# Performance work log

Measured on AMD Instinct MI355X. Metric: run time of the kernel, lower is better.

The kernel has to match this reference:

```python
import jax, jax.numpy as jnp
import numpy as np

M1, M2, M3 = 16, 16, 3  # Fourier mode truncation (modes3 hard-coded to 3 in torch __init__)


def setup_inputs() -> dict:
    key = jax.random.key(0)
    k0, k1, k2, k3, k4 = jax.random.split(key, 5)
    B, Ci, Co, T, X, P = 8, 32, 32, 128, 256, 3
    scale = 1.0 / (Ci * Co)
    x = jax.random.normal(k0, (B, Ci, T, X, P), dtype=jnp.float32)
    w1_re = scale * jax.random.uniform(k1, (Ci, Co, M1, M2, M3), dtype=jnp.float32)
    w1_im = scale * jax.random.uniform(k2, (Ci, Co, M1, M2, M3), dtype=jnp.float32)
    w2_re = scale * jax.random.uniform(k3, (Ci, Co, M1, M2, M3), dtype=jnp.float32)
    w2_im = scale * jax.random.uniform(k4, (Ci, Co, M1, M2, M3), dtype=jnp.float32)
    return {"x": x, "w1_re": w1_re, "w1_im": w1_im, "w2_re": w2_re, "w2_im": w2_im}


def reference(x, w1_re, w1_im, w2_re, w2_im):
    # x: [B, Ci, T, X, P] -- pipes pre-stacked along last dim (method == 34 branch)
    B, Ci, T, X, P = x.shape
    Co = w1_re.shape[1]
    w1 = (w1_re + 1j * w1_im).astype(jnp.complex64)
    w2 = (w2_re + 1j * w2_im).astype(jnp.complex64)

    x_ft = jnp.fft.rfftn(x, axes=(2, 3, 4))          # [B, Ci, T, X, P//2+1]
    z = min(x_ft.shape[4], M3)                       # torch: z_dim = min(x_ft.shape[4], modes3)

    # low-x / low-y corner
    coeff1 = jnp.zeros((B, Ci, M1, M2, M3), jnp.complex64)
    coeff1 = coeff1.at[..., :z].set(x_ft[:, :, :M1, :M2, :z])
    blk1 = jnp.einsum('bixyz,ioxyz->boxyz', coeff1, w1)

    # high-x / low-y corner
    coeff2 = jnp.zeros((B, Ci, M1, M2, M3), jnp.complex64)
    coeff2 = coeff2.at[..., :z].set(x_ft[:, :, -M1:, :M2, :z])
    blk2 = jnp.einsum('bixyz,ioxyz->boxyz', coeff2, w2)

    out_ft = jnp.zeros((B, Co, T, X, P), jnp.complex64)
    out_ft = out_ft.at[:, :, :M1, :M2, :M3].set(blk1)
    out_ft = out_ft.at[:, :, -M1:, :M2, :M3].set(blk2)

    # irfftn with s=(T, X, P) crops last axis to P//2+1 coeffs, matching torch semantics
    out = jnp.fft.irfftn(out_ft, s=(T, X, P), axes=(-3, -2, -1))  # [B, Co, T, X, P] float32
    return out
```

## Files before the change

### kernel.cpp

```cpp
#include <hip/hip_runtime.h>
#include <math.h>

typedef float2 F2;

__device__ __forceinline__ F2 cmul(F2 a, F2 b) {
    return make_float2(a.x * b.x - a.y * b.y, a.x * b.y + a.y * b.x);
}
__device__ __forceinline__ F2 cmac(F2 acc, F2 a, F2 b) {
    acc.x += a.x * b.x - a.y * b.y;
    acc.y += a.x * b.y + a.y * b.x;
    return acc;
}

#define TWO_PI 6.283185307179586f
#define SQRT3_2 0.8660254037844386f
#define SQRT3 1.7320508075688772f

__device__ constexpr float TW16X[16] = {
    1.f,  0.923879533f,  0.707106781f,  0.382683432f,  0.f, -0.382683432f,
    -0.707106781f, -0.923879533f, -1.f, -0.923879533f, -0.707106781f,
    -0.382683432f, 0.f,  0.382683432f,  0.707106781f,  0.923879533f};
__device__ constexpr float TW16Y[16] = {
    0.f, -0.382683432f, -0.707106781f, -0.923879533f, -1.f, -0.923879533f,
    -0.707106781f, -0.382683432f, 0.f,  0.382683432f,  0.707106781f,
    0.923879533f,  1.f,  0.923879533f,  0.707106781f,  0.382683432f};

__global__ __launch_bounds__(256) void k1_fwd_x(const float* __restrict__ x,
                                                F2* __restrict__ y) {
    __shared__ float xp0[8][260];
    __shared__ F2    xp1[8][260];
    __shared__ F2    tw[256];
    __shared__ F2    part[1024];
    const int tid = threadIdx.x;
    const int blk = blockIdx.x;

    {
        float sv, cv;
        sincosf(-TWO_PI * (float)tid * (1.0f / 256.0f), &sv, &cv);
        tw[tid] = make_float2(cv, sv);
    }
#pragma unroll
    for (int j = 0; j < 8; ++j) {
        int item = tid + 256 * j;
        int row = item >> 8, xx = item & 255;
        const float* src = x + ((size_t)(blk * 8 + row) * 256 + xx) * 3;
        float a = src[0], b = src[1], c = src[2];
        xp0[row][xx] = a + b + c;
        xp1[row][xx] = make_float2(a - 0.5f * (b + c), SQRT3_2 * (c - b));
    }
    __syncthreads();

    const int kz = tid >> 7, rr = (tid >> 4) & 7, kxg = (tid >> 2) & 3, c = tid & 3;
    const float sgn = (kxg & 1) ? -1.0f : 1.0f;

    const F2 c01 = tw[(32 * kxg) & 255];
    const F2 c02 = tw[(64 * kxg) & 255];
    const F2 c03 = tw[(96 * kxg) & 255];
    const F2 f1 = tw[(4 * c) & 255];
    const F2 f2 = tw[(8 * c) & 255];
    const F2 f3 = tw[(12 * c) & 255];

    F2 T0[8], T1[8];
    if (kz == 0) {
        const float* r0 = xp0[rr];
#pragma unroll
        for (int b = 0; b < 8; ++b) {
            int x0 = c + 4 * b;
            float s0 = fmaf(sgn, r0[x0 + 128], r0[x0]);
            float s1 = fmaf(sgn, r0[x0 + 160], r0[x0 + 32]);
            float s2 = fmaf(sgn, r0[x0 + 192], r0[x0 + 64]);
            float s3 = fmaf(sgn, r0[x0 + 224], r0[x0 + 96]);
            F2 p1 = make_float2(s1 * c01.x, s1 * c01.y);
            F2 p2 = make_float2(s2 * c02.x, s2 * c02.y);
            F2 p3 = make_float2(s3 * c03.x, s3 * c03.y);
            T0[b] = make_float2(s0 + p1.x + p2.x + p3.x, p1.y + p2.y + p3.y);
            T1[b] = make_float2(s0 - p1.x + p2.x - p3.x, -p1.y + p2.y - p3.y);
        }
    } else {
        const F2* r1 = xp1[rr];
#pragma unroll
        for (int b = 0; b < 8; ++b) {
            int x0 = c + 4 * b;
            F2 a0 = r1[x0],      b0 = r1[x0 + 128];
            F2 a1 = r1[x0 + 32], b1 = r1[x0 + 160];
            F2 a2 = r1[x0 + 64], b2 = r1[x0 + 192];
            F2 a3 = r1[x0 + 96], b3 = r1[x0 + 224];
            F2 s0 = make_float2(fmaf(sgn, b0.x, a0.x), fmaf(sgn, b0.y, a0.y));
            F2 s1 = make_float2(fmaf(sgn, b1.x, a1.x), fmaf(sgn, b1.y, a1.y));
            F2 s2 = make_float2(fmaf(sgn, b2.x, a2.x), fmaf(sgn, b2.y, a2.y));
            F2 s3 = make_float2(fmaf(sgn, b3.x, a3.x), fmaf(sgn, b3.y, a3.y));
            F2 p1 = cmul(s1, c01);
            F2 p2 = cmul(s2, c02);
            F2 p3 = cmul(s3, c03);
            T0[b] = make_float2(s0.x + p1.x + p2.x + p3.x, s0.y + p1.y + p2.y + p3.y);
            T1[b] = make_float2(s0.x - p1.x + p2.x - p3.x, s0.y - p1.y + p2.y - p3.y);
        }
    }

    F2 acc0 = make_float2(0.f, 0.f), acc1 = acc0, acc2 = acc0, acc3 = acc0;
#pragma unroll
    for (int b = 0; b < 8; ++b) {
        F2 tb = tw[(kxg * (c + 4 * b)) & 255];
        F2 q0 = cmul(tb, T0[b]);
        F2 q1 = cmul(tb, T1[b]);
        acc0.x += q0.x; acc0.y += q0.y;
        {
            const float Cx = TW16X[(2 * b) & 15], Cy = TW16Y[(2 * b) & 15];
            acc2.x += q0.x * Cx - q0.y * Cy;
            acc2.y += q0.x * Cy + q0.y * Cx;
        }
        {
            const float Cx = TW16X[b & 15], Cy = TW16Y[b & 15];
            acc1.x += q1.x * Cx - q1.y * Cy;
            acc1.y += q1.x * Cy + q1.y * Cx;
        }
        {
            const float Cx = TW16X[(3 * b) & 15], Cy = TW16Y[(3 * b) & 15];
            acc3.x += q1.x * Cx - q1.y * Cy;
            acc3.y += q1.x * Cy + q1.y * Cx;
        }
    }
    acc1 = cmul(acc1, f1);
    acc2 = cmul(acc2, f2);
    acc3 = cmul(acc3, f3);

    {
        const int base = (((rr * 2 + kz) * 16 + kxg) << 2) + c;
        part[base]       = acc0;
        part[base + 16]  = acc1;
        part[base + 32]  = acc2;
        part[base + 48]  = acc3;
    }
    __syncthreads();
    {
        int rr2 = tid >> 5, kz2 = (tid >> 4) & 1, kx2 = tid & 15;
        const F2* p = &part[((rr2 * 2 + kz2) * 16 + kx2) << 2];
        F2 r = p[0];
        r.x += p[1].x + p[2].x + p[3].x;
        r.y += p[1].y + p[2].y + p[3].y;
        y[((size_t)(blk * 8 + rr2) * 2 + kz2) * 16 + kx2] = r;
    }
}

__global__ __launch_bounds__(256) void k2a_fwd_t(const F2* __restrict__ y,
                                                 F2* __restrict__ xft) {
    __shared__ F2 yL[128][16];
    const int tid = threadIdx.x;
    const int bi = blockIdx.x >> 1, kz = blockIdx.x & 1;
#pragma unroll
    for (int j = 0; j < 8; ++j) {
        int item = tid + 256 * j;
        int t = item >> 4, kx = item & 15;
        yL[t][kx] = y[((size_t)(bi * 128 + t) * 2 + kz) * 16 + kx];
    }
    __syncthreads();

    const int kx = tid & 15, sg = tid >> 4;
    F2 rotA = make_float2(1.f, 0.f), rotB = make_float2(1.f, 0.f), stepA, stepB;
    sincosf(-TWO_PI * (float)sg * (1.0f / 128.0f), &stepA.y, &stepA.x);
    sincosf(-TWO_PI * (float)(112 + sg) * (1.0f / 128.0f), &stepB.y, &stepB.x);
    F2 accA = make_float2(0.f, 0.f), accB = make_float2(0.f, 0.f);
#pragma unroll 8
    for (int t = 0; t < 128; ++t) {
        F2 v = yL[t][kx];
        accA = cmac(accA, v, rotA);
        accB = cmac(accB, v, rotB);
        rotA = cmul(rotA, stepA);
        rotB = cmul(rotB, stepB);
    }
    const int b = bi >> 5, i = bi & 31;
    xft[(((size_t)(b * 32 + sg) * 2 + kz) * 16 + kx) * 32 + i] = accA;
    xft[(((size_t)(b * 32 + (16 + sg)) * 2 + kz) * 16 + kx) * 32 + i] = accB;
}

__global__ __launch_bounds__(256) void k2b_mix(const F2* __restrict__ xft,
                                               const float* __restrict__ w1re,
                                               const float* __restrict__ w1im,
                                               const float* __restrict__ w2re,
                                               const float* __restrict__ w2im,
                                               F2* __restrict__ blkout) {
    __shared__ F2 xL[512];
    __shared__ F2 wcL[2][32][32];
    const int tid = threadIdx.x;
    const int s = blockIdx.x >> 4, kx = blockIdx.x & 15;
#pragma unroll
    for (int j = 0; j < 2; ++j) {
        int item = tid + 256 * j;
        int b = item >> 6, kz = (item >> 5) & 1, i = item & 31;
        xL[item] = xft[(((size_t)(b * 32 + s) * 2 + kz) * 16 + kx) * 32 + i];
    }
    const float* bre = (s < 16) ? w1re : w2re;
    const float* bim = (s < 16) ? w1im : w2im;
    const int m1 = s & 15;
#pragma unroll
    for (int j = 0; j < 4; ++j) {
        int iop = tid + 256 * j;
        int i = iop >> 5, o = iop & 31;
        size_t g = (((size_t)(i * 32 + o) * 16 + m1) * 16 + kx) * 3;
        wcL[0][i][o] = make_float2(bre[g], bim[g]);
        wcL[1][i][o] = make_float2(bre[g + 1], bim[g + 1]);
    }
    __syncthreads();

    const int b = tid >> 5, o = tid & 31;
#pragma unroll
    for (int kz = 0; kz < 2; ++kz) {
        F2 acc = make_float2(0.f, 0.f);
#pragma unroll 8
        for (int i = 0; i < 32; ++i) {
            F2 xv = xL[(b * 2 + kz) * 32 + i];
            F2 wv = wcL[kz][i][o];
            acc.x += xv.x * wv.x - xv.y * wv.y;
            acc.y += xv.x * wv.y + xv.y * wv.x;
        }
        blkout[(((size_t)(b * 32 + o) * 32 + s) * 2 + kz) * 16 + kx] = acc;
    }
}

__global__ __launch_bounds__(256) void k2c_inv_t(const F2* __restrict__ blkin,
                                                 F2* __restrict__ h) {
    __shared__ F2 bL[1024];
    const int tid = threadIdx.x;
    const int bo = blockIdx.x >> 2, tc = blockIdx.x & 3;
#pragma unroll
    for (int j = 0; j < 4; ++j) {
        int item = tid + 256 * j;
        bL[item] = blkin[(size_t)bo * 1024 + item];
    }
    __syncthreads();

    const int col = tid & 31, tl = tid >> 5;
    F2 accA[4], accB[4], w[4], stp[4];
#pragma unroll
    for (int q = 0; q < 4; ++q) {
        accA[q] = make_float2(0.f, 0.f);
        accB[q] = make_float2(0.f, 0.f);
        w[q] = make_float2(1.f, 0.f);
        int t = 32 * tc + tl + 8 * q;
        sincosf(TWO_PI * (float)t * (1.0f / 128.0f), &stp[q].y, &stp[q].x);
    }
#pragma unroll 4
    for (int sp = 0; sp < 16; ++sp) {
        F2 bA = bL[sp * 32 + col];
        F2 bB = bL[(16 + sp) * 32 + col];
#pragma unroll
        for (int q = 0; q < 4; ++q) {
            accA[q] = cmac(accA[q], bA, w[q]);
            accB[q] = cmac(accB[q], bB, w[q]);
            w[q] = cmul(w[q], stp[q]);
        }
    }
    F2 phase;
    sincosf(-TWO_PI * (float)tl * (1.0f / 8.0f), &phase.y, &phase.x);
#pragma unroll
    for (int q = 0; q < 4; ++q) {
        int t = 32 * tc + tl + 8 * q;
        F2 r = cmac(accA[q], phase, accB[q]);
        h[((size_t)bo * 128 + t) * 32 + col] = r;
    }
}

__global__ __launch_bounds__(256) void k3_inv_x(const F2* __restrict__ h,
                                                float* __restrict__ out) {
    __shared__ F2 hL[64];
    __shared__ float oL[1536];
    const int tid = threadIdx.x;
    const int blk = blockIdx.x;
    if (tid < 64) hL[tid] = h[(size_t)blk * 64 + tid];
    __syncthreads();

    const int rr = tid >> 7, x = tid & 127;
    const F2* hrow = &hL[rr * 32];
    F2 w = make_float2(1.f, 0.f), r;
    sincosf(TWO_PI * (float)x * (1.0f / 256.0f), &r.y, &r.x);
    float e0 = 0.f, o0 = 0.f;
    F2 e1 = make_float2(0.f, 0.f), o1 = make_float2(0.f, 0.f);
#pragma unroll
    for (int k2 = 0; k2 < 8; ++k2) {
        {
            F2 h0 = hrow[2 * k2], h1 = hrow[16 + 2 * k2];
            e0 += h0.x * w.x - h0.y * w.y;
            e1.x += h1.x * w.x - h1.y * w.y;
            e1.y += h1.x * w.y + h1.y * w.x;
            w = cmul(w, r);
        }
        {
            F2 h0 = hrow[2 * k2 + 1], h1 = hrow[16 + 2 * k2 + 1];
            o0 += h0.x * w.x - h0.y * w.y;
            o1.x += h1.x * w.x - h1.y * w.y;
            o1.y += h1.x * w.y + h1.y * w.x;
            w = cmul(w, r);
        }
    }
    const float n = 1.0f / 98304.0f;
    float* o = &oL[rr * 768];
    {
        float g0 = e0 + o0, g1r = e1.x + o1.x, g1i = e1.y + o1.y;
        o[x * 3 + 0] = n * (g0 + 2.f * g1r);
        o[x * 3 + 1] = n * (g0 - g1r - SQRT3 * g1i);
        o[x * 3 + 2] = n * (g0 - g1r + SQRT3 * g1i);
    }
    {
        float g0 = e0 - o0, g1r = e1.x - o1.x, g1i = e1.y - o1.y;
        int xb = x + 128;
        o[xb * 3 + 0] = n * (g0 + 2.f * g1r);
        o[xb * 3 + 1] = n * (g0 - g1r - SQRT3 * g1i);
        o[xb * 3 + 2] = n * (g0 - g1r + SQRT3 * g1i);
    }
    __syncthreads();
    {
        float4* dst = (float4*)(out + (size_t)blk * 1536);
        const float4* src = (const float4*)oL;
        dst[tid] = src[tid];
        if (tid < 128) dst[tid + 256] = src[tid + 256];
    }
}

extern "C" void kernel_launch(void* const* d_in, const int* in_sizes, int n_in,
                              void* d_out, int out_size, void* d_ws, size_t ws_size,
                              hipStream_t stream) {
    const float* x    = (const float*)d_in[0];
    const float* w1re = (const float*)d_in[1];
    const float* w1im = (const float*)d_in[2];
    const float* w2re = (const float*)d_in[3];
    const float* w2im = (const float*)d_in[4];
    float* out = (float*)d_out;

    F2* y   = (F2*)d_ws;
    F2* xft = y + 1048576;
    F2* bk  = xft + 262144;
    F2* h   = bk + 262144;

    hipLaunchKernelGGL(k1_fwd_x,  dim3(4096),  dim3(256), 0, stream, x, y);
    hipLaunchKernelGGL(k2a_fwd_t, dim3(512),   dim3(256), 0, stream, y, xft);
    hipLaunchKernelGGL(k2b_mix,   dim3(512),   dim3(256), 0, stream, xft,
                       w1re, w1im, w2re, w2im, bk);
    hipLaunchKernelGGL(k2c_inv_t, dim3(1024),  dim3(256), 0, stream, bk, h);
    hipLaunchKernelGGL(k3_inv_x,  dim3(16384), dim3(256), 0, stream, h, out);
}
```

Measured before the change: 253.7 us.

## Fuse inverse T-DFT and inverse X/P-DFT kernels through shared memory

Merges the inverse time-axis DFT kernel and the inverse x/p-axis kernel into one kernel. The intermediate h tile stays in shared memory instead of making a round trip through global memory, and one launch is dropped. Each block now produces 32 time rows in four rounds, with extra syncs between rounds. The grid drops from 16384 small blocks to 1024 blocks, and shared memory use rises to about 40KB per block, which may lower occupancy.

```diff
diff --git a/kernel.cpp b/kernel.cpp
--- a/kernel.cpp
+++ b/kernel.cpp
@@ -217,11 +217,14 @@
     }
 }
 
-__global__ __launch_bounds__(256) void k2c_inv_t(const F2* __restrict__ blkin,
-                                                 F2* __restrict__ h) {
+__global__ __launch_bounds__(256) void k23_inv_tx(const F2* __restrict__ blkin,
+                                                  float* __restrict__ out) {
     __shared__ F2 bL[1024];
+    __shared__ F2 hT[32][32];
+    __shared__ __align__(16) float oL[8][768];
     const int tid = threadIdx.x;
     const int bo = blockIdx.x >> 2, tc = blockIdx.x & 3;
+
 #pragma unroll
     for (int j = 0; j < 4; ++j) {
         int item = tid + 256 * j;
@@ -229,90 +232,88 @@
     }
     __syncthreads();
 
-    const int col = tid & 31, tl = tid >> 5;
-    F2 accA[4], accB[4], w[4], stp[4];
-#pragma unroll
-    for (int q = 0; q < 4; ++q) {
-        accA[q] = make_float2(0.f, 0.f);
-        accB[q] = make_float2(0.f, 0.f);
-        w[q] = make_float2(1.f, 0.f);
-        int t = 32 * tc + tl + 8 * q;
-        sincosf(TWO_PI * (float)t * (1.0f / 128.0f), &stp[q].y, &stp[q].x);
-    }
+    {
+        const int col = tid & 31, tl = tid >> 5;
+        F2 accA[4], accB[4], w[4], stp[4];
+#pragma unroll
+        for (int q = 0; q < 4; ++q) {
+            accA[q] = make_float2(0.f, 0.f);
+            accB[q] = make_float2(0.f, 0.f);
+            w[q] = make_float2(1.f, 0.f);
+            int t = 32 * tc + tl + 8 * q;
+            sincosf(TWO_PI * (float)t * (1.0f / 128.0f), &stp[q].y, &stp[q].x);
+        }
 #pragma unroll 4
-    for (int sp = 0; sp < 16; ++sp) {
-        F2 bA = bL[sp * 32 + col];
-        F2 bB = bL[(16 + sp) * 32 + col];
+        for (int sp = 0; sp < 16; ++sp) {
+            F2 bA = bL[sp * 32 + col];
+            F2 bB = bL[(16 + sp) * 32 + col];
+#pragma unroll
+            for (int q = 0; q < 4; ++q) {
+                accA[q] = cmac(accA[q], bA, w[q]);
+                accB[q] = cmac(accB[q], bB, w[q]);
+                w[q] = cmul(w[q], stp[q]);
+            }
+        }
+        F2 phase;
+        sincosf(-TWO_PI * (float)tl * (1.0f / 8.0f), &phase.y, &phase.x);
 #pragma unroll
         for (int q = 0; q < 4; ++q) {
-            accA[q] = cmac(accA[q], bA, w[q]);
-            accB[q] = cmac(accB[q], bB, w[q]);
-            w[q] = cmul(w[q], stp[q]);
-        }
-    }
-    F2 phase;
-    sincosf(-TWO_PI * (float)tl * (1.0f / 8.0f), &phase.y, &phase.x);
-#pragma unroll
-    for (int q = 0; q < 4; ++q) {
-        int t = 32 * tc + tl + 8 * q;
-        F2 r = cmac(accA[q], phase, accB[q]);
-        h[((size_t)bo * 128 + t) * 32 + col] = r;
-    }
-}
-
-__global__ __launch_bounds__(256) void k3_inv_x(const F2* __restrict__ h,
-                                                float* __restrict__ out) {
-    __shared__ F2 hL[64];
-    __shared__ float oL[1536];
-    const int tid = threadIdx.x;
-    const int blk = blockIdx.x;
-    if (tid < 64) hL[tid] = h[(size_t)blk * 64 + tid];
-    __syncthreads();
-
-    const int rr = tid >> 7, x = tid & 127;
-    const F2* hrow = &hL[rr * 32];
-    F2 w = make_float2(1.f, 0.f), r;
-    sincosf(TWO_PI * (float)x * (1.0f / 256.0f), &r.y, &r.x);
-    float e0 = 0.f, o0 = 0.f;
-    F2 e1 = make_float2(0.f, 0.f), o1 = make_float2(0.f, 0.f);
-#pragma unroll
-    for (int k2 = 0; k2 < 8; ++k2) {
+            hT[tl + 8 * q][col] = cmac(accA[q], phase, accB[q]);
+        }
+    }
+    __syncthreads();
+
+    const int xg = tid & 31, tl2 = tid >> 5;
+    const float n = 1.0f / 98304.0f;
+    for (int rd = 0; rd < 4; ++rd) {
+        const F2* hrow = &hT[rd * 8 + tl2][0];
+        float* o = oL[tl2];
+#pragma unroll
+        for (int j = 0; j < 4; ++j) {
+            const int x = xg + 32 * j;
+            F2 w = make_float2(1.f, 0.f), r;
+            sincosf(TWO_PI * (float)x * (1.0f / 256.0f), &r.y, &r.x);
+            float e0 = 0.f, o0 = 0.f;
+            F2 e1 = make_float2(0.f, 0.f), o1 = make_float2(0.f, 0.f);
+#pragma unroll
+            for (int k2 = 0; k2 < 8; ++k2) {
+                {
+                    F2 h0 = hrow[2 * k2], h1 = hrow[16 + 2 * k2];
+                    e0 += h0.x * w.x - h0.y * w.y;
+                    e1.x += h1.x * w.x - h1.y * w.y;
+                    e1.y += h1.x * w.y + h1.y * w.x;
+                    w = cmul(w, r);
+                }
+                {
+                    F2 h0 = hrow[2 * k2 + 1], h1 = hrow[16 + 2 * k2 + 1];
+                    o0 += h0.x * w.x - h0.y * w.y;
+                    o1.x += h1.x * w.x - h1.y * w.y;
+                    o1.y += h1.x * w.y + h1.y * w.x;
+                    w = cmul(w, r);
+                }
+            }
+            {
+                float g0 = e0 + o0, g1r = e1.x + o1.x, g1i = e1.y + o1.y;
+                o[x * 3 + 0] = n * (g0 + 2.f * g1r);
+                o[x * 3 + 1] = n * (g0 - g1r - SQRT3 * g1i);
+                o[x * 3 + 2] = n * (g0 - g1r + SQRT3 * g1i);
+            }
+            {
+                float g0 = e0 - o0, g1r = e1.x - o1.x, g1i = e1.y - o1.y;
+                int xb = x + 128;
+                o[xb * 3 + 0] = n * (g0 + 2.f * g1r);
+                o[xb * 3 + 1] = n * (g0 - g1r - SQRT3 * g1i);
+                o[xb * 3 + 2] = n * (g0 - g1r + SQRT3 * g1i);
+            }
+        }
+        __syncthreads();
         {
-            F2 h0 = hrow[2 * k2], h1 = hrow[16 + 2 * k2];
-            e0 += h0.x * w.x - h0.y * w.y;
-            e1.x += h1.x * w.x - h1.y * w.y;
-            e1.y += h1.x * w.y + h1.y * w.x;
-            w = cmul(w, r);
-        }
-        {
-            F2 h0 = hrow[2 * k2 + 1], h1 = hrow[16 + 2 * k2 + 1];
-            o0 += h0.x * w.x - h0.y * w.y;
-            o1.x += h1.x * w.x - h1.y * w.y;
-            o1.y += h1.x * w.y + h1.y * w.x;
-            w = cmul(w, r);
-        }
-    }
-    const float n = 1.0f / 98304.0f;
-    float* o = &oL[rr * 768];
-    {
-        float g0 = e0 + o0, g1r = e1.x + o1.x, g1i = e1.y + o1.y;
-        o[x * 3 + 0] = n * (g0 + 2.f * g1r);
-        o[x * 3 + 1] = n * (g0 - g1r - SQRT3 * g1i);
-        o[x * 3 + 2] = n * (g0 - g1r + SQRT3 * g1i);
-    }
-    {
-        float g0 = e0 - o0, g1r = e1.x - o1.x, g1i = e1.y - o1.y;
-        int xb = x + 128;
-        o[xb * 3 + 0] = n * (g0 + 2.f * g1r);
-        o[xb * 3 + 1] = n * (g0 - g1r - SQRT3 * g1i);
-        o[xb * 3 + 2] = n * (g0 - g1r + SQRT3 * g1i);
-    }
-    __syncthreads();
-    {
-        float4* dst = (float4*)(out + (size_t)blk * 1536);
-        const float4* src = (const float4*)oL;
-        dst[tid] = src[tid];
-        if (tid < 128) dst[tid + 256] = src[tid + 256];
+            float4* dst = (float4*)(out + ((size_t)bo * 128 + 32 * tc + 8 * rd) * 768);
+            const float4* src = (const float4*)oL;
+#pragma unroll
+            for (int k = 0; k < 6; ++k) dst[tid + 256 * k] = src[tid + 256 * k];
+        }
+        __syncthreads();
     }
 }
 
@@ -329,12 +330,10 @@
     F2* y   = (F2*)d_ws;
     F2* xft = y + 1048576;
     F2* bk  = xft + 262144;
-    F2* h   = bk + 262144;
-
-    hipLaunchKernelGGL(k1_fwd_x,  dim3(4096),  dim3(256), 0, stream, x, y);
-    hipLaunchKernelGGL(k2a_fwd_t, dim3(512),   dim3(256), 0, stream, y, xft);
-    hipLaunchKernelGGL(k2b_mix,   dim3(512),   dim3(256), 0, stream, xft,
+
+    hipLaunchKernelGGL(k1_fwd_x,   dim3(4096), dim3(256), 0, stream, x, y);
+    hipLaunchKernelGGL(k2a_fwd_t,  dim3(512),  dim3(256), 0, stream, y, xft);
+    hipLaunchKernelGGL(k2b_mix,    dim3(512),  dim3(256), 0, stream, xft,
                        w1re, w1im, w2re, w2im, bk);
-    hipLaunchKernelGGL(k2c_inv_t, dim3(1024),  dim3(256), 0, stream, bk, h);
-    hipLaunchKernelGGL(k3_inv_x,  dim3(16384), dim3(256), 0, stream, h, out);
-}
+    hipLaunchKernelGGL(k23_inv_tx, dim3(1024), dim3(256), 0, stream, bk, out);
+}
```

New measurement: 283.0 us. 1.12x slower.
